# Kernel tuning notes

Hardware: AMD Instinct MI355X
Metric: run time of the kernel (lower is better)

## Reference

```python
import jax, jax.numpy as jnp
import numpy as np

EPS = 1e-9
SPREAD_WEIGHT = 0.1
QUAD_WEIGHT = 1.0

N_NODES = 200000
N_EDGES = 12800000
DIM = 128


def to_uhg_space(x):
    # dim > 2: truncate to first 2 features, append homogeneous 1 -> [..., 3]
    ones = jnp.ones((*x.shape[:-1], 1), dtype=x.dtype)
    return jnp.concatenate([x[..., :2], ones], axis=-1)


def uhg_inner(a, b):
    # -<spatial,spatial> + time*time, keepdim
    return -jnp.sum(a[..., :-1] * b[..., :-1], axis=-1, keepdims=True) + a[..., -1:] * b[..., -1:]


def uhg_quadrance(a, b):
    aa = uhg_inner(a, a)
    bb = uhg_inner(b, b)
    ab = uhg_inner(a, b)
    num = ab * ab - aa * bb
    den = aa * bb
    safe = jnp.maximum(jnp.abs(den), EPS) * jnp.sign(den)
    return (num / safe).squeeze(-1)


# spread has the identical formula, applied to lines instead of points
uhg_spread = uhg_quadrance


def setup_inputs() -> dict:
    key = jax.random.key(0)
    k1, k2 = jax.random.split(key)
    z = jax.random.normal(k1, (N_NODES, DIM), dtype=jnp.float32)
    edge_index = jax.random.randint(k2, (2, N_EDGES), 0, N_NODES, dtype=jnp.int32)
    return {"z": z, "edge_index": edge_index}


def reference(z, edge_index):
    z_uhg = to_uhg_space(z)                      # [N, 3]
    src, dst = edge_index[0], edge_index[1]
    # proximity: quadrance over all edges (gather + fused elementwise + mean)
    quad = uhg_quadrance(z_uhg[src], z_uhg[dst])  # [E]
    proximity_loss = quad.mean()
    # compactness: quadrance of every node to the origin [0,0,1]
    origin = jnp.zeros((1, 3), dtype=z.dtype).at[:, -1].set(1.0)
    compactness_loss = uhg_quadrance(z_uhg, origin).mean()
    # lines: vectorized cross product of each point with the origin
    lines = jnp.cross(z_uhg, origin)              # [N, 3]
    # spread over the first min(10, E) edges only (as in the original)
    n_sp = min(10, edge_index.shape[1])
    sp = uhg_spread(lines[src[:n_sp]], lines[dst[:n_sp]])
    spread_loss = sp.mean()
    loss = QUAD_WEIGHT * (proximity_loss + compactness_loss) + SPREAD_WEIGHT * spread_loss
    return loss
```

## Files before the change

### kernel.cpp

```cpp
#include <hip/hip_runtime.h>
#include <hip/hip_bf16.h>

#define UHG_EPS 1e-9
#define ZDIM 128

#define EDGE_BLOCKS 1024
#define NODE_BLOCKS 1024
#define BLOCK 256

#define PART_SHIFT 13
#define PART_SIZE (1 << PART_SHIFT)
#define P_MAX 25
#define NBINS_MAX (P_MAX * P_MAX)
#define RING 48
#define CHUNK 32
#define FCHUNK 16
#define SCAT_BLOCKS 256
#define SBLOCK 1024
#define BBLOCK 1024
#define SENTINEL 0xFFFFFFFFu
#define OVGUARD 1024
#define GPAD 16

#define PROX_OFF 0
#define COMP_OFF (16 * 1024)
#define GCUR_OFF (32 * 1024)
#define TABLE_OFF (128 * 1024)

typedef float vfloat2 __attribute__((ext_vector_type(2)));
typedef int vint4 __attribute__((ext_vector_type(4)));
typedef unsigned uvec4 __attribute__((ext_vector_type(4)));

__device__ vfloat2 llvm_amdgcn_raw_buffer_load_v2f32(vint4 rsrc, int voffset, int soffset,
                                                     int cpol) __asm("llvm.amdgcn.raw.buffer.load.v2f32");

__device__ __forceinline__ vint4 make_srd(const void* base, unsigned int bytes) {
    union { const void* p; unsigned int w[2]; } pb;
    pb.p = base;
    vint4 r;
    r.x = (int)pb.w[0];
    r.y = (int)pb.w[1];
    r.z = (int)bytes;
    r.w = 0x00020000;
    return r;
}


__device__ __forceinline__ double safe_den(double den) {
    return copysign(fmax(fabs(den), UHG_EPS), den);
}

__device__ __forceinline__ double quad_xy(vfloat2 a, vfloat2 b) {
    double xa = a.x, ya = a.y, xb = b.x, yb = b.y;
    double aa = 1.0 - (xa * xa + ya * ya);
    double bb = 1.0 - (xb * xb + yb * yb);
    double ab = 1.0 - (xa * xb + ya * yb);
    double den = aa * bb;
    double num = ab * ab - den;
    return num / safe_den(den);
}

__device__ __forceinline__ double wave_reduce(double v) {
    v += __shfl_down(v, 32);
    v += __shfl_down(v, 16);
    v += __shfl_down(v, 8);
    v += __shfl_down(v, 4);
    v += __shfl_down(v, 2);
    v += __shfl_down(v, 1);
    return v;
}

__device__ __forceinline__ double block_reduce(double v, double* sh) {
    int lane = threadIdx.x & 63;
    int wid = threadIdx.x >> 6;
    v = wave_reduce(v);
    if (lane == 0) sh[wid] = v;
    __syncthreads();
    double r = 0.0;
    if (wid == 0) {
        int nw = (int)(blockDim.x >> 6);
        r = (lane < nw) ? sh[lane] : 0.0;
        r += __shfl_down(r, 8);
        r += __shfl_down(r, 4);
        r += __shfl_down(r, 2);
        r += __shfl_down(r, 1);
    }
    __syncthreads();
    return r;
}


__global__ __launch_bounds__(BLOCK) void node_kernel(const float* __restrict__ z,
                                                     vfloat2* __restrict__ table,
                                                     double* __restrict__ comp_partials, int N) {
    __shared__ double sh[16];
    const vfloat2* zp = (const vfloat2*)z;
    double local = 0.0;
    for (int i = blockIdx.x * BLOCK + threadIdx.x; i < N; i += NODE_BLOCKS * BLOCK) {
        vfloat2 v = zp[(size_t)i * (ZDIM / 2)];
        if (table) table[i] = v;
        double x = v.x, y = v.y;
        double aa = 1.0 - (x * x + y * y);
        local += (1.0 - aa) / safe_den(aa);
    }
    double tot = block_reduce(local, sh);
    if (threadIdx.x == 0) comp_partials[blockIdx.x] = tot;
}

__global__ __launch_bounds__(SBLOCK) void scatter_kernel(const float* __restrict__ z,
                                                         vfloat2* __restrict__ table,
                                                         double* __restrict__ comp_partials,
                                                         int N,
                                                         const int* __restrict__ src,
                                                         const int* __restrict__ dst, int E,
                                                         int P, int nbins,
                                                         unsigned* __restrict__ gcur,
                                                         unsigned* __restrict__ gbins,
                                                         int bincap) {
    __shared__ unsigned cnt[NBINS_MAX];
    __shared__ unsigned sstart[NBINS_MAX];
    __shared__ __align__(16) unsigned stage[NBINS_MAX][RING];
    __shared__ double sh[16];
    const int tid = threadIdx.x;
    const unsigned botlim = (unsigned)(bincap - OVGUARD);

    for (int b = tid; b < nbins; b += SBLOCK) {
        cnt[b] = 0u;
        sstart[b] = 0u;
    }
    __syncthreads();

    {
        const vfloat2* zp = (const vfloat2*)z;
        long n0 = (long)blockIdx.x * N / SCAT_BLOCKS;
        long n1 = (long)(blockIdx.x + 1) * N / SCAT_BLOCKS;
        double comp = 0.0;
        for (long i = n0 + tid; i < n1; i += SBLOCK) {
            vfloat2 v = zp[(size_t)i * (ZDIM / 2)];
            table[i] = v;
            double x = v.x, y = v.y;
            double aa = 1.0 - (x * x + y * y);
            comp += (1.0 - aa) / safe_den(aa);
        }
        double tot = block_reduce(comp, sh);
        if (tid == 0) comp_partials[blockIdx.x] = tot;
    }

    auto ovf = [&](int b, unsigned v) {
        unsigned hp = atomicAdd(&gcur[(size_t)(nbins + b) * GPAD], 1u);
        if (hp < (unsigned)OVGUARD)
            gbins[(size_t)b * bincap + (bincap - 1 - (int)hp)] = v;
    };

    auto write_seg16 = [&](int b, unsigned s, unsigned* out) {
        const unsigned* sp = &stage[b][s];
        *(uvec4*)(out + 0) = *(const uvec4*)(sp + 0);
        *(uvec4*)(out + 4) = *(const uvec4*)(sp + 4);
        *(uvec4*)(out + 8) = *(const uvec4*)(sp + 8);
        *(uvec4*)(out + 12) = *(const uvec4*)(sp + 12);
    };
    auto ovf_seg16 = [&](int b, unsigned s, unsigned cnt16) {
        for (unsigned j = 0; j < cnt16; ++j) ovf(b, stage[b][s + j]);
    };

    auto flush_bins = [&](bool final_pad) {
        int b = tid;
        if (b < nbins) {
            unsigned n = cnt[b];
            unsigned st = sstart[b];
            unsigned m = n < (unsigned)RING ? n : (unsigned)RING;
            while (m >= (unsigned)CHUNK) {
                unsigned s0 = st;
                unsigned s1 = st + 16 >= (unsigned)RING ? st + 16 - RING : st + 16;
                unsigned pos = atomicAdd(&gcur[(size_t)b * GPAD], (unsigned)CHUNK);
                if (pos + CHUNK <= botlim) {
                    unsigned* out = gbins + (size_t)b * bincap + pos;
                    write_seg16(b, s0, out);
                    write_seg16(b, s1, out + 16);
                } else {
                    ovf_seg16(b, s0, 16u);
                    ovf_seg16(b, s1, 16u);
                }
                st = st + 32 >= (unsigned)RING ? st + 32 - RING : st + 32;
                m -= (unsigned)CHUNK;
            }
            if (final_pad) {
                while (m >= (unsigned)FCHUNK) {
                    unsigned pos = atomicAdd(&gcur[(size_t)b * GPAD], (unsigned)FCHUNK);
                    if (pos + FCHUNK <= botlim) {
                        write_seg16(b, st, gbins + (size_t)b * bincap + pos);
                    } else {
                        ovf_seg16(b, st, 16u);
                    }
                    st = st + 16 >= (unsigned)RING ? st + 16 - RING : st + 16;
                    m -= (unsigned)FCHUNK;
                }
                if (m > 0) {
                    for (unsigned j = m; j < (unsigned)FCHUNK; ++j) stage[b][st + j] = SENTINEL;
                    unsigned pos = atomicAdd(&gcur[(size_t)b * GPAD], (unsigned)FCHUNK);
                    if (pos + FCHUNK <= botlim) {
                        write_seg16(b, st, gbins + (size_t)b * bincap + pos);
                    } else {
                        ovf_seg16(b, st, m);
                    }
                    st = st + 16 >= (unsigned)RING ? st + 16 - RING : st + 16;
                    m = 0;
                }
            }
            cnt[b] = m;
            sstart[b] = st;
        }
    };

    const long nv4 = (long)E / 4;
    long g0 = (long)blockIdx.x * nv4 / SCAT_BLOCKS;
    long g1 = (long)(blockIdx.x + 1) * nv4 / SCAT_BLOCKS;
    const vint4* s4 = (const vint4*)src;
    const vint4* d4 = (const vint4*)dst;
    long nbatch = (g1 - g0 + SBLOCK - 1) / SBLOCK;

    long i = g0 + tid;
    vint4 cs = {}, cd = {};
    if (i < g1) {
        cs = __builtin_nontemporal_load(s4 + i);
        cd = __builtin_nontemporal_load(d4 + i);
    }
    for (long k = 0; k < nbatch; ++k) {
        bool valid = i < g1;
        vint4 s = cs, d = cd;
        long inext = i + SBLOCK;
        if (inext < g1) {
            cs = __builtin_nontemporal_load(s4 + inext);
            cd = __builtin_nontemporal_load(d4 + inext);
        }
        __builtin_amdgcn_sched_barrier(0);
        if (valid) {
            int bn0 = (s.x >> PART_SHIFT) * P + (d.x >> PART_SHIFT);
            int bn1 = (s.y >> PART_SHIFT) * P + (d.y >> PART_SHIFT);
            int bn2 = (s.z >> PART_SHIFT) * P + (d.z >> PART_SHIFT);
            int bn3 = (s.w >> PART_SHIFT) * P + (d.w >> PART_SHIFT);
            unsigned vl0 = (unsigned)(s.x & (PART_SIZE - 1)) | ((unsigned)(d.x & (PART_SIZE - 1)) << PART_SHIFT);
            unsigned vl1 = (unsigned)(s.y & (PART_SIZE - 1)) | ((unsigned)(d.y & (PART_SIZE - 1)) << PART_SHIFT);
            unsigned vl2 = (unsigned)(s.z & (PART_SIZE - 1)) | ((unsigned)(d.z & (PART_SIZE - 1)) << PART_SHIFT);
            unsigned vl3 = (unsigned)(s.w & (PART_SIZE - 1)) | ((unsigned)(d.w & (PART_SIZE - 1)) << PART_SHIFT);
            unsigned st0 = sstart[bn0], st1 = sstart[bn1], st2 = sstart[bn2], st3 = sstart[bn3];
            unsigned sl0 = atomicAdd(&cnt[bn0], 1u);
            unsigned sl1 = atomicAdd(&cnt[bn1], 1u);
            unsigned sl2 = atomicAdd(&cnt[bn2], 1u);
            unsigned sl3 = atomicAdd(&cnt[bn3], 1u);
            unsigned p0 = st0 + sl0; if (p0 >= (unsigned)RING) p0 -= (unsigned)RING;
            unsigned p1 = st1 + sl1; if (p1 >= (unsigned)RING) p1 -= (unsigned)RING;
            unsigned p2 = st2 + sl2; if (p2 >= (unsigned)RING) p2 -= (unsigned)RING;
            unsigned p3 = st3 + sl3; if (p3 >= (unsigned)RING) p3 -= (unsigned)RING;
            if (sl0 < (unsigned)RING) stage[bn0][p0] = vl0; else ovf(bn0, vl0);
            if (sl1 < (unsigned)RING) stage[bn1][p1] = vl1; else ovf(bn1, vl1);
            if (sl2 < (unsigned)RING) stage[bn2][p2] = vl2; else ovf(bn2, vl2);
            if (sl3 < (unsigned)RING) stage[bn3][p3] = vl3; else ovf(bn3, vl3);
        }
        __syncthreads();
        flush_bins(false);
        __syncthreads();
        i = inext;
    }
    if (blockIdx.x == SCAT_BLOCKS - 1) {
        for (long e = 4 * nv4 + tid; e < E; e += SBLOCK) {
            int s = src[e], d = dst[e];
            int bn = (s >> PART_SHIFT) * P + (d >> PART_SHIFT);
            unsigned vl = (unsigned)(s & (PART_SIZE - 1)) |
                          ((unsigned)(d & (PART_SIZE - 1)) << PART_SHIFT);
            unsigned st = sstart[bn];
            unsigned sl = atomicAdd(&cnt[bn], 1u);
            unsigned p = st + sl; if (p >= (unsigned)RING) p -= (unsigned)RING;
            if (sl < (unsigned)RING) stage[bn][p] = vl; else ovf(bn, vl);
        }
    }
    __syncthreads();
    flush_bins(true);
}

__global__ __launch_bounds__(BBLOCK) void binned_edge_kernel(const vfloat2* __restrict__ table,
                                                             int N, int P,
                                                             const unsigned* __restrict__ gcur,
                                                             const unsigned* __restrict__ gbins,
                                                             int bincap,
                                                             double* __restrict__ prox_partials) {
    __shared__ vfloat2 pts[2][PART_SIZE];
    __shared__ double sh[16];
    const int bin = blockIdx.x >> 1;
    const int half = blockIdx.x & 1;
    const int sp = bin / P, dp = bin % P;
    const int tid = threadIdx.x;
    const int nbins = P * P;
    const unsigned botlim = (unsigned)(bincap - OVGUARD);

    for (int j = tid; j < PART_SIZE; j += BBLOCK) {
        int gs = (sp << PART_SHIFT) + j;
        int gd = (dp << PART_SHIFT) + j;
        vfloat2 zv = {0.0f, 0.0f};
        pts[0][j] = (gs < N) ? table[gs] : zv;
        pts[1][j] = (gd < N) ? table[gd] : zv;
    }
    __syncthreads();

    unsigned lo = gcur[(size_t)bin * GPAD];
    if (lo > botlim) lo = botlim;
    unsigned hi = gcur[(size_t)(nbins + bin) * GPAD];
    if (hi > (unsigned)OVGUARD) hi = (unsigned)OVGUARD;
    const unsigned* eb = gbins + (size_t)bin * bincap;

    unsigned h0 = (lo >> 1) & ~3u;
    unsigned rs = half ? h0 : 0u;
    unsigned re = half ? lo : h0;

    double local = 0.0;
    unsigned ng = (re - rs) >> 2;
    const uvec4* eb4 = (const uvec4*)(eb + rs);
    unsigned i = tid;
    bool have = i < ng;
    uvec4 cur = {};
    if (have) cur = __builtin_nontemporal_load(eb4 + i);
    while (have) {
        unsigned in2 = i + BBLOCK;
        bool hn = in2 < ng;
        uvec4 nxt = {};
        if (hn) nxt = __builtin_nontemporal_load(eb4 + in2);
        __builtin_amdgcn_sched_barrier(0);
        vfloat2 a0 = pts[0][cur.x & (PART_SIZE - 1u)], b0 = pts[1][(cur.x >> PART_SHIFT) & (PART_SIZE - 1u)];
        vfloat2 a1 = pts[0][cur.y & (PART_SIZE - 1u)], b1 = pts[1][(cur.y >> PART_SHIFT) & (PART_SIZE - 1u)];
        vfloat2 a2 = pts[0][cur.z & (PART_SIZE - 1u)], b2 = pts[1][(cur.z >> PART_SHIFT) & (PART_SIZE - 1u)];
        vfloat2 a3 = pts[0][cur.w & (PART_SIZE - 1u)], b3 = pts[1][(cur.w >> PART_SHIFT) & (PART_SIZE - 1u)];
        if (cur.x != SENTINEL) local += quad_xy(a0, b0);
        if (cur.y != SENTINEL) local += quad_xy(a1, b1);
        if (cur.z != SENTINEL) local += quad_xy(a2, b2);
        if (cur.w != SENTINEL) local += quad_xy(a3, b3);
        cur = nxt;
        i = in2;
        have = hn;
    }
    for (unsigned j = rs + (ng << 2) + tid; j < re; j += BBLOCK) {
        unsigned v = eb[j];
        if (v != SENTINEL)
            local += quad_xy(pts[0][v & (PART_SIZE - 1u)],
                             pts[1][(v >> PART_SHIFT) & (PART_SIZE - 1u)]);
    }
    if (half) {
        for (unsigned j = tid; j < hi; j += BBLOCK) {
            unsigned v = eb[bincap - 1 - (int)j];
            local += quad_xy(pts[0][v & (PART_SIZE - 1u)],
                             pts[1][(v >> PART_SHIFT) & (PART_SIZE - 1u)]);
        }
    }
    double tot = block_reduce(local, sh);
    if (tid == 0) prox_partials[blockIdx.x] = tot;
}

#define GATHER8(dsta, i0, i1)                                                   \
    dsta[0] = llvm_amdgcn_raw_buffer_load_v2f32(srd, (i0).x << SHIFT, 0, 1);    \
    dsta[1] = llvm_amdgcn_raw_buffer_load_v2f32(srd, (i0).y << SHIFT, 0, 1);    \
    dsta[2] = llvm_amdgcn_raw_buffer_load_v2f32(srd, (i0).z << SHIFT, 0, 1);    \
    dsta[3] = llvm_amdgcn_raw_buffer_load_v2f32(srd, (i0).w << SHIFT, 0, 1);    \
    dsta[4] = llvm_amdgcn_raw_buffer_load_v2f32(srd, (i1).x << SHIFT, 0, 1);    \
    dsta[5] = llvm_amdgcn_raw_buffer_load_v2f32(srd, (i1).y << SHIFT, 0, 1);    \
    dsta[6] = llvm_amdgcn_raw_buffer_load_v2f32(srd, (i1).z << SHIFT, 0, 1);    \
    dsta[7] = llvm_amdgcn_raw_buffer_load_v2f32(srd, (i1).w << SHIFT, 0, 1);

template <int COMPACT>
__global__ __launch_bounds__(BLOCK) void edge_kernel(const vint4* __restrict__ src4,
                                                     const vint4* __restrict__ dst4, int nvec,
                                                     const int* __restrict__ src,
                                                     const int* __restrict__ dst, int E,
                                                     const void* __restrict__ xy, int N,
                                                     double* __restrict__ prox_partials) {
    __shared__ double sh[16];
    double local = 0.0;
    int tid = blockIdx.x * BLOCK + threadIdx.x;
    const int gstride = EDGE_BLOCKS * BLOCK;
    const int SHIFT = COMPACT ? 3 : 9;

    vint4 srd = make_srd(xy, COMPACT ? (unsigned int)N * 8u : (unsigned int)N * 512u);

    int nvec2 = nvec / 2;
    int v0 = tid;
    bool p0 = v0 < nvec2;
    int v1 = v0 + gstride;
    bool p1 = v1 < nvec2;

    vint4 is0 = {}, is1 = {}, id0 = {}, id1 = {};
    vfloat2 ca[8] = {}, cb[8] = {};
    vfloat2 na[8] = {}, nb[8] = {};

    if (p0) {
        vint4 s0 = __builtin_nontemporal_load(src4 + 2 * (long)v0);
        vint4 s1 = __builtin_nontemporal_load(src4 + 2 * (long)v0 + 1);
        vint4 d0 = __builtin_nontemporal_load(dst4 + 2 * (long)v0);
        vint4 d1 = __builtin_nontemporal_load(dst4 + 2 * (long)v0 + 1);
        GATHER8(ca, s0, s1);
        GATHER8(cb, d0, d1);
    }
    if (p1) {
        is0 = __builtin_nontemporal_load(src4 + 2 * (long)v1);
        is1 = __builtin_nontemporal_load(src4 + 2 * (long)v1 + 1);
        id0 = __builtin_nontemporal_load(dst4 + 2 * (long)v1);
        id1 = __builtin_nontemporal_load(dst4 + 2 * (long)v1 + 1);
    }

    while (p0) {
        if (p1) {
            GATHER8(na, is0, is1);
            GATHER8(nb, id0, id1);
        }
        int v2 = v1 + gstride;
        bool p2 = v2 < nvec2;
        if (p2) {
            is0 = __builtin_nontemporal_load(src4 + 2 * (long)v2);
            is1 = __builtin_nontemporal_load(src4 + 2 * (long)v2 + 1);
            id0 = __builtin_nontemporal_load(dst4 + 2 * (long)v2);
            id1 = __builtin_nontemporal_load(dst4 + 2 * (long)v2 + 1);
        }
        __builtin_amdgcn_sched_barrier(0);
#pragma unroll
        for (int i = 0; i < 8; ++i) local += quad_xy(ca[i], cb[i]);
#pragma unroll
        for (int i = 0; i < 8; ++i) { ca[i] = na[i]; cb[i] = nb[i]; }
        p0 = p1;
        v1 = v2;
        p1 = p2;
    }

    for (int e = 8 * nvec2 + tid; e < E; e += gstride) {
        vfloat2 a = llvm_amdgcn_raw_buffer_load_v2f32(srd, src[e] << SHIFT, 0, 1);
        vfloat2 b = llvm_amdgcn_raw_buffer_load_v2f32(srd, dst[e] << SHIFT, 0, 1);
        local += quad_xy(a, b);
    }
    double tot = block_reduce(local, sh);
    if (threadIdx.x == 0) prox_partials[blockIdx.x] = tot;
}

__global__ __launch_bounds__(BLOCK) void finalize_kernel(const int* __restrict__ src,
                                                         const int* __restrict__ dst,
                                                         const float* __restrict__ z,
                                                         const double* __restrict__ prox_partials,
                                                         int nprox,
                                                         const double* __restrict__ comp_partials,
                                                         int ncomp,
                                                         float* __restrict__ out, int N, int E) {
    __shared__ double sh[16];
    int t = threadIdx.x;

    double pl = 0.0;
    for (int i = t; i < nprox; i += BLOCK) pl += prox_partials[i];
    double prox = block_reduce(pl, sh);

    double cl = 0.0;
    for (int i = t; i < ncomp; i += BLOCK) cl += comp_partials[i];
    double comp = block_reduce(cl, sh);

    int n_sp = E < 10 ? E : 10;
    double sl = 0.0;
    if (t < n_sp) {
        int s = src[t], d = dst[t];
        double xa = z[(size_t)s * ZDIM], ya = z[(size_t)s * ZDIM + 1];
        double xb = z[(size_t)d * ZDIM], yb = z[(size_t)d * ZDIM + 1];
        double aa = -(ya * ya + xa * xa);
        double bb = -(yb * yb + xb * xb);
        double ab = -(ya * yb + xa * xb);
        double den = aa * bb;
        sl = (ab * ab - den) / safe_den(den);
    }
    double spread = block_reduce(sl, sh);

    if (t == 0) {
        double loss = prox / (double)E + comp / (double)N;
        if (n_sp > 0) loss += 0.1 * (spread / (double)n_sp);
        out[0] = (float)loss;
    }
}


extern "C" void kernel_launch(void* const* d_in, const int* in_sizes, int n_in,
                              void* d_out, int out_size, void* d_ws, size_t ws_size,
                              hipStream_t stream) {
    const float* z = (const float*)d_in[0];
    const int* edge_index = (const int*)d_in[1];
    float* out = (float*)d_out;

    const int N = in_sizes[0] / ZDIM;
    const int E = in_sizes[1] / 2;
    const int* src = edge_index;
    const int* dst = edge_index + (size_t)E;

    double* prox_partials = (double*)((char*)d_ws + PROX_OFF);
    double* comp_partials = (double*)((char*)d_ws + COMP_OFF);
    unsigned* gcur = (unsigned*)((char*)d_ws + GCUR_OFF);
    vfloat2* table = (vfloat2*)((char*)d_ws + TABLE_OFF);
    bool use_table = ws_size >= TABLE_OFF + (size_t)N * sizeof(vfloat2);

    const int P = (N + PART_SIZE - 1) >> PART_SHIFT;
    const int nbins = P * P;
    size_t gbins_off = TABLE_OFF + (((size_t)N * 8 + 255) & ~(size_t)255);
    bool use_binned = false;
    unsigned* gbins = nullptr;
    int bincap = 0;
    if (use_table && P >= 1 && P <= P_MAX && nbins <= NBINS_MAX && E > nbins * 64 &&
        ws_size > gbins_off) {
        int mean = E / nbins;
        int cap_want = (mean + 4608 + OVGUARD + 31) & ~31;
        int need_min = mean + 3072 + OVGUARD;
        size_t avail = ws_size - gbins_off;
        int cap_fit = (int)((avail / ((size_t)nbins * 4)) & ~(size_t)31);
        bincap = cap_fit < cap_want ? cap_fit : cap_want;
        if (bincap >= need_min) {
            use_binned = true;
            gbins = (unsigned*)((char*)d_ws + gbins_off);
        }
    }

    if (use_binned) {
        hipMemsetAsync(gcur, 0, (size_t)2 * nbins * GPAD * sizeof(unsigned), stream);
        scatter_kernel<<<SCAT_BLOCKS, SBLOCK, 0, stream>>>(z, table, comp_partials, N,
                                                           src, dst, E, P, nbins, gcur,
                                                           gbins, bincap);
        binned_edge_kernel<<<2 * nbins, BBLOCK, 0, stream>>>(table, N, P, gcur, gbins, bincap,
                                                             prox_partials);
        finalize_kernel<<<1, BLOCK, 0, stream>>>(src, dst, z, prox_partials, 2 * nbins,
                                                 comp_partials, SCAT_BLOCKS,
                                                 out, N, E);
    } else {
        node_kernel<<<NODE_BLOCKS, BLOCK, 0, stream>>>(z, use_table ? table : nullptr,
                                                       comp_partials, N);
        int nvec = E / 4;
        if (use_table) {
            edge_kernel<1><<<EDGE_BLOCKS, BLOCK, 0, stream>>>((const vint4*)src,
                                                              (const vint4*)dst, nvec, src, dst,
                                                              E, table, N, prox_partials);
        } else {
            edge_kernel<0><<<EDGE_BLOCKS, BLOCK, 0, stream>>>((const vint4*)src,
                                                              (const vint4*)dst, nvec, src, dst,
                                                              E, z, N, prox_partials);
        }
        finalize_kernel<<<1, BLOCK, 0, stream>>>(src, dst, z, prox_partials, EDGE_BLOCKS,
                                                 comp_partials, NODE_BLOCKS, out, N, E);
    }
}
```

Measured before the change: 267.7 us.

## Split per-bin global cursors into per-slice segments to cut atomic contention

Each bin's global buffer is divided into four slices, one per group of scatter blocks, each with its own atomic cursor, so fewer blocks contend on the same counter. The binned edge kernel now walks the slices (two per half) instead of splitting one contiguous range. Unused slice tails are filled with sentinels when a slice overflows, and the overflow guard shrinks. The cost is more cursor memory, a larger workspace offset, and the loss of the software-prefetch double buffering in the consumer loop.

```diff
diff --git a/kernel.cpp b/kernel.cpp
--- a/kernel.cpp
+++ b/kernel.cpp
@@ -17,15 +17,17 @@
 #define FCHUNK 16
 #define SCAT_BLOCKS 256
 #define SBLOCK 1024
+#define SLICES 4
+#define SLICE_BLOCKS (SCAT_BLOCKS / SLICES)
 #define BBLOCK 1024
 #define SENTINEL 0xFFFFFFFFu
-#define OVGUARD 1024
+#define OVGUARD 512
 #define GPAD 16
 
 #define PROX_OFF 0
 #define COMP_OFF (16 * 1024)
 #define GCUR_OFF (32 * 1024)
-#define TABLE_OFF (128 * 1024)
+#define TABLE_OFF (576 * 1024)
 
 typedef float vfloat2 __attribute__((ext_vector_type(2)));
 typedef int vint4 __attribute__((ext_vector_type(4)));
@@ -116,13 +118,14 @@
                                                          int P, int nbins,
                                                          unsigned* __restrict__ gcur,
                                                          unsigned* __restrict__ gbins,
-                                                         int bincap) {
+                                                         int scap) {
     __shared__ unsigned cnt[NBINS_MAX];
     __shared__ unsigned sstart[NBINS_MAX];
     __shared__ __align__(16) unsigned stage[NBINS_MAX][RING];
     __shared__ double sh[16];
     const int tid = threadIdx.x;
-    const unsigned botlim = (unsigned)(bincap - OVGUARD);
+    const int slice = blockIdx.x / SLICE_BLOCKS;
+    const int bincap = SLICES * scap + OVGUARD;
 
     for (int b = tid; b < nbins; b += SBLOCK) {
         cnt[b] = 0u;
@@ -147,7 +150,7 @@
     }
 
     auto ovf = [&](int b, unsigned v) {
-        unsigned hp = atomicAdd(&gcur[(size_t)(nbins + b) * GPAD], 1u);
+        unsigned hp = atomicAdd(&gcur[(size_t)(nbins * SLICES + b) * GPAD], 1u);
         if (hp < (unsigned)OVGUARD)
             gbins[(size_t)b * bincap + (bincap - 1 - (int)hp)] = v;
     };
@@ -162,22 +165,28 @@
     auto ovf_seg16 = [&](int b, unsigned s, unsigned cnt16) {
         for (unsigned j = 0; j < cnt16; ++j) ovf(b, stage[b][s + j]);
     };
+    auto fill_gap = [&](int b, unsigned pos, unsigned* sbase) {
+        if (pos < (unsigned)scap)
+            for (unsigned j = pos; j < (unsigned)scap; ++j) sbase[j] = SENTINEL;
+    };
 
     auto flush_bins = [&](bool final_pad) {
         int b = tid;
         if (b < nbins) {
+            unsigned* sbase = gbins + (size_t)b * bincap + (size_t)slice * scap;
+            unsigned* cur = &gcur[(size_t)(b * SLICES + slice) * GPAD];
             unsigned n = cnt[b];
             unsigned st = sstart[b];
             unsigned m = n < (unsigned)RING ? n : (unsigned)RING;
             while (m >= (unsigned)CHUNK) {
                 unsigned s0 = st;
                 unsigned s1 = st + 16 >= (unsigned)RING ? st + 16 - RING : st + 16;
-                unsigned pos = atomicAdd(&gcur[(size_t)b * GPAD], (unsigned)CHUNK);
-                if (pos + CHUNK <= botlim) {
-                    unsigned* out = gbins + (size_t)b * bincap + pos;
-                    write_seg16(b, s0, out);
-                    write_seg16(b, s1, out + 16);
+                unsigned pos = atomicAdd(cur, (unsigned)CHUNK);
+                if (pos + CHUNK <= (unsigned)scap) {
+                    write_seg16(b, s0, sbase + pos);
+                    write_seg16(b, s1, sbase + pos + 16);
                 } else {
+                    fill_gap(b, pos, sbase);
                     ovf_seg16(b, s0, 16u);
                     ovf_seg16(b, s1, 16u);
                 }
@@ -186,10 +195,11 @@
             }
             if (final_pad) {
                 while (m >= (unsigned)FCHUNK) {
-                    unsigned pos = atomicAdd(&gcur[(size_t)b * GPAD], (unsigned)FCHUNK);
-                    if (pos + FCHUNK <= botlim) {
-                        write_seg16(b, st, gbins + (size_t)b * bincap + pos);
+                    unsigned pos = atomicAdd(cur, (unsigned)FCHUNK);
+                    if (pos + FCHUNK <= (unsigned)scap) {
+                        write_seg16(b, st, sbase + pos);
                     } else {
+                        fill_gap(b, pos, sbase);
                         ovf_seg16(b, st, 16u);
                     }
                     st = st + 16 >= (unsigned)RING ? st + 16 - RING : st + 16;
@@ -197,10 +207,11 @@
                 }
                 if (m > 0) {
                     for (unsigned j = m; j < (unsigned)FCHUNK; ++j) stage[b][st + j] = SENTINEL;
-                    unsigned pos = atomicAdd(&gcur[(size_t)b * GPAD], (unsigned)FCHUNK);
-                    if (pos + FCHUNK <= botlim) {
-                        write_seg16(b, st, gbins + (size_t)b * bincap + pos);
+                    unsigned pos = atomicAdd(cur, (unsigned)FCHUNK);
+                    if (pos + FCHUNK <= (unsigned)scap) {
+                        write_seg16(b, st, sbase + pos);
                     } else {
+                        fill_gap(b, pos, sbase);
                         ovf_seg16(b, st, m);
                     }
                     st = st + 16 >= (unsigned)RING ? st + 16 - RING : st + 16;
@@ -282,7 +293,7 @@
                                                              int N, int P,
                                                              const unsigned* __restrict__ gcur,
                                                              const unsigned* __restrict__ gbins,
-                                                             int bincap,
+                                                             int scap,
                                                              double* __restrict__ prox_partials) {
     __shared__ vfloat2 pts[2][PART_SIZE];
     __shared__ double sh[16];
@@ -291,7 +302,7 @@
     const int sp = bin / P, dp = bin % P;
     const int tid = threadIdx.x;
     const int nbins = P * P;
-    const unsigned botlim = (unsigned)(bincap - OVGUARD);
+    const int bincap = SLICES * scap + OVGUARD;
 
     for (int j = tid; j < PART_SIZE; j += BBLOCK) {
         int gs = (sp << PART_SHIFT) + j;
@@ -302,48 +313,38 @@
     }
     __syncthreads();
 
-    unsigned lo = gcur[(size_t)bin * GPAD];
-    if (lo > botlim) lo = botlim;
-    unsigned hi = gcur[(size_t)(nbins + bin) * GPAD];
-    if (hi > (unsigned)OVGUARD) hi = (unsigned)OVGUARD;
     const unsigned* eb = gbins + (size_t)bin * bincap;
-
-    unsigned h0 = (lo >> 1) & ~3u;
-    unsigned rs = half ? h0 : 0u;
-    unsigned re = half ? lo : h0;
-
     double local = 0.0;
-    unsigned ng = (re - rs) >> 2;
-    const uvec4* eb4 = (const uvec4*)(eb + rs);
-    unsigned i = tid;
-    bool have = i < ng;
-    uvec4 cur = {};
-    if (have) cur = __builtin_nontemporal_load(eb4 + i);
-    while (have) {
-        unsigned in2 = i + BBLOCK;
-        bool hn = in2 < ng;
-        uvec4 nxt = {};
-        if (hn) nxt = __builtin_nontemporal_load(eb4 + in2);
-        __builtin_amdgcn_sched_barrier(0);
-        vfloat2 a0 = pts[0][cur.x & (PART_SIZE - 1u)], b0 = pts[1][(cur.x >> PART_SHIFT) & (PART_SIZE - 1u)];
-        vfloat2 a1 = pts[0][cur.y & (PART_SIZE - 1u)], b1 = pts[1][(cur.y >> PART_SHIFT) & (PART_SIZE - 1u)];
-        vfloat2 a2 = pts[0][cur.z & (PART_SIZE - 1u)], b2 = pts[1][(cur.z >> PART_SHIFT) & (PART_SIZE - 1u)];
-        vfloat2 a3 = pts[0][cur.w & (PART_SIZE - 1u)], b3 = pts[1][(cur.w >> PART_SHIFT) & (PART_SIZE - 1u)];
-        if (cur.x != SENTINEL) local += quad_xy(a0, b0);
-        if (cur.y != SENTINEL) local += quad_xy(a1, b1);
-        if (cur.z != SENTINEL) local += quad_xy(a2, b2);
-        if (cur.w != SENTINEL) local += quad_xy(a3, b3);
-        cur = nxt;
-        i = in2;
-        have = hn;
-    }
-    for (unsigned j = rs + (ng << 2) + tid; j < re; j += BBLOCK) {
-        unsigned v = eb[j];
-        if (v != SENTINEL)
-            local += quad_xy(pts[0][v & (PART_SIZE - 1u)],
-                             pts[1][(v >> PART_SHIFT) & (PART_SIZE - 1u)]);
+
+    const int s0 = half ? SLICES / 2 : 0;
+    const int s1 = half ? SLICES : SLICES / 2;
+    for (int s = s0; s < s1; ++s) {
+        unsigned len = gcur[(size_t)(bin * SLICES + s) * GPAD];
+        if (len > (unsigned)scap) len = (unsigned)scap;
+        const unsigned* sb = eb + (size_t)s * scap;
+        unsigned ng = len >> 2;
+        const uvec4* sb4 = (const uvec4*)sb;
+        for (unsigned i = tid; i < ng; i += BBLOCK) {
+            uvec4 c = __builtin_nontemporal_load(sb4 + i);
+            vfloat2 a0 = pts[0][c.x & (PART_SIZE - 1u)], b0 = pts[1][(c.x >> PART_SHIFT) & (PART_SIZE - 1u)];
+            vfloat2 a1 = pts[0][c.y & (PART_SIZE - 1u)], b1 = pts[1][(c.y >> PART_SHIFT) & (PART_SIZE - 1u)];
+            vfloat2 a2 = pts[0][c.z & (PART_SIZE - 1u)], b2 = pts[1][(c.z >> PART_SHIFT) & (PART_SIZE - 1u)];
+            vfloat2 a3 = pts[0][c.w & (PART_SIZE - 1u)], b3 = pts[1][(c.w >> PART_SHIFT) & (PART_SIZE - 1u)];
+            if (c.x != SENTINEL) local += quad_xy(a0, b0);
+            if (c.y != SENTINEL) local += quad_xy(a1, b1);
+            if (c.z != SENTINEL) local += quad_xy(a2, b2);
+            if (c.w != SENTINEL) local += quad_xy(a3, b3);
+        }
+        for (unsigned j = (ng << 2) + tid; j < len; j += BBLOCK) {
+            unsigned v = sb[j];
+            if (v != SENTINEL)
+                local += quad_xy(pts[0][v & (PART_SIZE - 1u)],
+                                 pts[1][(v >> PART_SHIFT) & (PART_SIZE - 1u)]);
+        }
     }
     if (half) {
+        unsigned hi = gcur[(size_t)(nbins * SLICES + bin) * GPAD];
+        if (hi > (unsigned)OVGUARD) hi = (unsigned)OVGUARD;
         for (unsigned j = tid; j < hi; j += BBLOCK) {
             unsigned v = eb[bincap - 1 - (int)j];
             local += quad_xy(pts[0][v & (PART_SIZE - 1u)],
@@ -500,27 +501,29 @@
     size_t gbins_off = TABLE_OFF + (((size_t)N * 8 + 255) & ~(size_t)255);
     bool use_binned = false;
     unsigned* gbins = nullptr;
-    int bincap = 0;
+    int scap = 0;
     if (use_table && P >= 1 && P <= P_MAX && nbins <= NBINS_MAX && E > nbins * 64 &&
         ws_size > gbins_off) {
-        int mean = E / nbins;
-        int cap_want = (mean + 4608 + OVGUARD + 31) & ~31;
-        int need_min = mean + 3072 + OVGUARD;
+        int mean_slice = E / (nbins * SLICES);
+        int scap_want = (mean_slice + SLICE_BLOCKS * 8 + 224 + 31) & ~31;
+        int scap_min = mean_slice + SLICE_BLOCKS * 8 + 96;
         size_t avail = ws_size - gbins_off;
-        int cap_fit = (int)((avail / ((size_t)nbins * 4)) & ~(size_t)31);
-        bincap = cap_fit < cap_want ? cap_fit : cap_want;
-        if (bincap >= need_min) {
+        long per_bin_fit = (long)(avail / ((size_t)nbins * 4));
+        int scap_fit = (int)(((per_bin_fit - OVGUARD) / SLICES) & ~31L);
+        scap = scap_fit < scap_want ? scap_fit : scap_want;
+        if (scap >= scap_min) {
             use_binned = true;
             gbins = (unsigned*)((char*)d_ws + gbins_off);
         }
     }
 
     if (use_binned) {
-        hipMemsetAsync(gcur, 0, (size_t)2 * nbins * GPAD * sizeof(unsigned), stream);
+        hipMemsetAsync(gcur, 0, (size_t)(nbins * SLICES + nbins) * GPAD * sizeof(unsigned),
+                       stream);
         scatter_kernel<<<SCAT_BLOCKS, SBLOCK, 0, stream>>>(z, table, comp_partials, N,
                                                            src, dst, E, P, nbins, gcur,
-                                                           gbins, bincap);
-        binned_edge_kernel<<<2 * nbins, BBLOCK, 0, stream>>>(table, N, P, gcur, gbins, bincap,
+                                                           gbins, scap);
+        binned_edge_kernel<<<2 * nbins, BBLOCK, 0, stream>>>(table, N, P, gcur, gbins, scap,
                                                              prox_partials);
         finalize_kernel<<<1, BLOCK, 0, stream>>>(src, dst, z, prox_partials, 2 * nbins,
                                                  comp_partials, SCAT_BLOCKS,
```

Measured after the change: 283.2 us. 1.06x slower.
